# Kernel tuning notes

Hardware: AMD Instinct MI355X
Metric: run time of the kernel (lower is better)

Reference implementation:

```python
import jax, jax.numpy as jnp
import numpy as np

B, E, N = 8, 256, 32          # triples, padded edges per triple, neighbors per edge
D, RD = 512, 768              # graph_dim, relation-semantic dim
R = 2000                      # num relations
L = 2                         # relation-context layers
K = 8                         # top_k neighbor similarity
M, HEADS = 32, 8              # memory tokens, memory-attention heads
HLLM = 4096                   # llm hidden size
EPS = 1e-5


def _ln(x, g, b):
    mu = jnp.mean(x, -1, keepdims=True)
    var = jnp.mean(jnp.square(x - mu), -1, keepdims=True)
    return (x - mu) * jax.lax.rsqrt(var + EPS) * g + b


def setup_inputs() -> dict:
    key = jax.random.key(0)
    ks = iter(jax.random.split(key, 40))
    nrm = lambda shape, s=0.02: jax.random.normal(next(ks), shape, jnp.float32) * s
    return {
        'edge_rel_ids': jax.random.randint(next(ks), (B, E), 0, R, jnp.int32),
        'neighbor_rel_ids': jax.random.randint(next(ks), (B, E, N), 0, R, jnp.int32),
        'edge_mask': jnp.ones((B, E), jnp.float32),
        'rel_emb': nrm((R, RD), 1.0),
        'rp_w': nrm((D, RD)), 'rp_b': jnp.zeros((D,), jnp.float32),
        'ly_vw': nrm((L, D, D)), 'ly_vb': jnp.zeros((L, D), jnp.float32),
        'ly_ow': nrm((L, D, D)), 'ly_ob': jnp.zeros((L, D), jnp.float32),
        'ly_n1g': jnp.ones((L, D), jnp.float32), 'ly_n1b': jnp.zeros((L, D), jnp.float32),
        'ly_n2g': jnp.ones((L, D), jnp.float32), 'ly_n2b': jnp.zeros((L, D), jnp.float32),
        'ly_w1': nrm((L, 4 * D, D)), 'ly_b1': jnp.zeros((L, 4 * D), jnp.float32),
        'ly_w2': nrm((L, D, 4 * D)), 'ly_b2': jnp.zeros((L, D), jnp.float32),
        'mem_q': nrm((M, D)),
        't_qw': nrm((D, D)), 't_qb': jnp.zeros((D,), jnp.float32),
        't_kw': nrm((D, D)), 't_kb': jnp.zeros((D,), jnp.float32),
        't_vw': nrm((D, D)), 't_vb': jnp.zeros((D,), jnp.float32),
        't_ow': nrm((D, D)), 't_ob': jnp.zeros((D,), jnp.float32),
        'proj_w': nrm((HLLM, D)), 'proj_b': jnp.zeros((HLLM,), jnp.float32),
    }


def reference(edge_rel_ids, neighbor_rel_ids, edge_mask, rel_emb, rp_w, rp_b,
              ly_vw, ly_vb, ly_ow, ly_ob, ly_n1g, ly_n1b, ly_n2g, ly_n2b,
              ly_w1, ly_b1, ly_w2, ly_b2, mem_q,
              t_qw, t_qb, t_kw, t_kb, t_vw, t_vb, t_ow, t_ob, proj_w, proj_b):
    rel_vector = lambda ids: rel_emb[ids] @ rp_w.T + rp_b  # embedding gather + rel_proj
    rel_vec = rel_vector(edge_rel_ids)            # [B,E,D]
    neigh = rel_vector(neighbor_rel_ids)          # [B,E,N,D] dominant gather traffic
    # per-edge cosine similarity to neighbor relations, top-k mean aggregation
    rn = rel_vec / jnp.maximum(jnp.linalg.norm(rel_vec, axis=-1, keepdims=True), 1e-12)
    nn_ = neigh / jnp.maximum(jnp.linalg.norm(neigh, axis=-1, keepdims=True), 1e-12)
    sims = jnp.einsum('bend,bed->ben', nn_, rn)   # [B,E,N]
    _, top_idx = jax.lax.top_k(sims, K)           # [B,E,K]
    agg = jnp.take_along_axis(neigh, top_idx[..., None], axis=2).mean(axis=2)  # [B,E,D]
    # RelationContextLayer stack. Each layer attends from one edge-state token to a
    # single context token: softmax over one key is identically 1, so the MHA
    # reduces exactly to out_proj(v_proj(context)) -- same math as torch MHA here.
    states = rel_vec
    for l in range(L):
        attn = (agg @ ly_vw[l].T + ly_vb[l]) @ ly_ow[l].T + ly_ob[l]
        states = _ln(states + attn, ly_n1g[l], ly_n1b[l])
        ff = jax.nn.gelu(states @ ly_w1[l].T + ly_b1[l], approximate=False) @ ly_w2[l].T + ly_b2[l]
        states = _ln(states + ff, ly_n2g[l], ly_n2b[l])
        states = states * edge_mask[..., None]
    # GraphMemoryTokenizer: learned queries cross-attend over padded edge states
    dh = D // HEADS
    q = (mem_q @ t_qw.T + t_qb).reshape(M, HEADS, dh)
    k = (states @ t_kw.T + t_kb).reshape(B, E, HEADS, dh)
    v = (states @ t_vw.T + t_vb).reshape(B, E, HEADS, dh)
    scores = jnp.einsum('mhd,behd->bhme', q, k) / jnp.sqrt(jnp.asarray(dh, q.dtype))
    scores = jnp.where(edge_mask[:, None, None, :] == 0, jnp.finfo(scores.dtype).min, scores)
    attnw = jax.nn.softmax(scores, axis=-1)
    mem = jnp.einsum('bhme,behd->bmhd', attnw, v).reshape(B, M, D)
    mem = mem @ t_ow.T + t_ob
    no_edges = jnp.sum(edge_mask, axis=1) == 0    # rows with zero edges -> zero memory
    mem = jnp.where(no_edges[:, None, None], 0.0, mem)
    return mem @ proj_w.T + proj_b                # [B,M,HLLM]
```

## Files before the change

### kernel.cpp

```cpp
#include <hip/hip_runtime.h>
#include <hip/hip_bf16.h>
#include <math.h>

#define B_   8
#define E_   256
#define N_   32
#define D_   512
#define RD_  768
#define R_   2000
#define L_   2
#define K_   8
#define M_   32
#define H_   8
#define DH_  64
#define HL_  4096

typedef float f32x4 __attribute__((ext_vector_type(4)));
typedef __bf16 bf16x8 __attribute__((ext_vector_type(8)));
typedef const __attribute__((address_space(1))) void GVoid;
typedef __attribute__((address_space(3))) void LVoid;

__device__ __forceinline__ float gelu_exact(float x) {
    return 0.5f * x * (1.0f + erff(x * 0.70710678118654752f));
}
__device__ __forceinline__ unsigned short f2bf(float x) {
    return __hip_bfloat16_raw(__float2bfloat16(x)).x;
}

template <int TM, int TN, int ACT_GELU, int OUT_BF16, int HAS_BIAS, int FLAGS>
__global__ __launch_bounds__(256) void gemm_mfma(const unsigned short* __restrict__ A,
                                                 const unsigned short* __restrict__ W,
                                                 const float* __restrict__ bias,
                                                 void* __restrict__ Cv,
                                                 int M, int N, int K,
                                                 const float* __restrict__ rowflag) {
    constexpr int WTM = TM / 2, WTN = TN / 2;
    constexpr int RM = WTM / 16, RN = WTN / 16;
    constexpr int AI = TM / 32, BI = TN / 32;
    __shared__ __align__(16) unsigned short As[TM * 64];
    __shared__ __align__(16) unsigned short Bs[TN * 64];

    const int tid = threadIdx.x;
    const int wave = tid >> 6, lane = tid & 63;
    const int quad = lane >> 4, l16 = lane & 15;
    const int wm = wave >> 1, wn = wave & 1;
    const int bm = blockIdx.y * TM, bn = blockIdx.x * TN;
    const int sub = lane >> 3;
    const int cpr = (lane & 7) ^ sub;

    f32x4 acc[RM][RN];
#pragma unroll
    for (int i = 0; i < RM; i++)
#pragma unroll
        for (int j = 0; j < RN; j++) acc[i][j] = (f32x4){0.f, 0.f, 0.f, 0.f};

    for (int k0 = 0; k0 < K; k0 += 64) {
        __syncthreads();
#pragma unroll
        for (int i = 0; i < AI; i++) {
            int r0 = (wave * AI + i) * 8;
            const unsigned short* g = A + (size_t)(bm + r0 + sub) * K + k0 + cpr * 8;
            __builtin_amdgcn_global_load_lds((GVoid*)g, (LVoid*)&As[r0 * 64], 16, 0, 0);
        }
#pragma unroll
        for (int i = 0; i < BI; i++) {
            int r0 = (wave * BI + i) * 8;
            const unsigned short* g = W + (size_t)(bn + r0 + sub) * K + k0 + cpr * 8;
            __builtin_amdgcn_global_load_lds((GVoid*)g, (LVoid*)&Bs[r0 * 64], 16, 0, 0);
        }
        __syncthreads();
#pragma unroll
        for (int h = 0; h < 2; h++) {
            bf16x8 af[RM], bf[RN];
#pragma unroll
            for (int i = 0; i < RM; i++) {
                int r = wm * WTM + i * 16 + l16;
                int ch = (h * 4 + quad) ^ (r & 7);
                af[i] = *(const bf16x8*)&As[r * 64 + ch * 8];
            }
#pragma unroll
            for (int j = 0; j < RN; j++) {
                int r = wn * WTN + j * 16 + l16;
                int ch = (h * 4 + quad) ^ (r & 7);
                bf[j] = *(const bf16x8*)&Bs[r * 64 + ch * 8];
            }
#pragma unroll
            for (int i = 0; i < RM; i++)
#pragma unroll
                for (int j = 0; j < RN; j++)
                    acc[i][j] = __builtin_amdgcn_mfma_f32_16x16x32_bf16(af[i], bf[j], acc[i][j], 0, 0, 0);
        }
    }

#pragma unroll
    for (int i = 0; i < RM; i++) {
#pragma unroll
        for (int j = 0; j < RN; j++) {
            int c = bn + wn * WTN + j * 16 + l16;
            float bv = HAS_BIAS ? bias[c] : 0.f;
#pragma unroll
            for (int reg = 0; reg < 4; reg++) {
                int r = bm + wm * WTM + i * 16 + quad * 4 + reg;
                if (r < M) {
                    float v = acc[i][j][reg] + bv;
                    if (ACT_GELU) v = gelu_exact(v);
                    if (FLAGS) v *= rowflag[r >> 5];
                    if (OUT_BF16)
                        ((unsigned short*)Cv)[(size_t)r * N + c] = f2bf(v);
                    else
                        ((float*)Cv)[(size_t)r * N + c] = v;
                }
            }
        }
    }
}

__global__ __launch_bounds__(256) void projwfuse_kernel(
        const unsigned short* __restrict__ rel_bf, const unsigned short* __restrict__ rpw_bf,
        const float* __restrict__ rp_b, float* __restrict__ proj,
        const unsigned short* __restrict__ ow_bf, const unsigned short* __restrict__ vwT_bf,
        unsigned short* __restrict__ wfuse) {
    __shared__ __align__(16) unsigned short As[32 * 64];
    __shared__ __align__(16) unsigned short Bs[64 * 64];

    const unsigned short *A, *W;
    const float* bias;
    int Mg, Kg, bm, bn, obf;
    void* C;
    int t = blockIdx.x;
    if (t < 504) {
        A = rel_bf; W = rpw_bf; bias = rp_b; Mg = R_; Kg = RD_;
        C = proj; obf = 0; bn = (t & 7) * 64; bm = (t >> 3) * 32;
    } else {
        int u = t - 504, z = u >> 7, uu = u & 127;
        A = ow_bf + (size_t)z * 262144; W = vwT_bf + (size_t)z * 262144;
        bias = nullptr; Mg = 512; Kg = 512;
        C = wfuse + (size_t)z * 262144; obf = 1; bn = (uu & 7) * 64; bm = (uu >> 3) * 32;
    }

    const int tid = threadIdx.x;
    const int wave = tid >> 6, lane = tid & 63;
    const int quad = lane >> 4, l16 = lane & 15;
    const int wm = wave >> 1, wn = wave & 1;
    const int sub = lane >> 3;
    const int cpr = (lane & 7) ^ sub;

    f32x4 acc[2];
    acc[0] = (f32x4){0.f, 0.f, 0.f, 0.f};
    acc[1] = (f32x4){0.f, 0.f, 0.f, 0.f};

    for (int k0 = 0; k0 < Kg; k0 += 64) {
        __syncthreads();
        {
            int r0 = wave * 8;
            const unsigned short* g = A + (size_t)(bm + r0 + sub) * Kg + k0 + cpr * 8;
            __builtin_amdgcn_global_load_lds((GVoid*)g, (LVoid*)&As[r0 * 64], 16, 0, 0);
        }
#pragma unroll
        for (int i = 0; i < 2; i++) {
            int r0 = (wave * 2 + i) * 8;
            const unsigned short* g = W + (size_t)(bn + r0 + sub) * Kg + k0 + cpr * 8;
            __builtin_amdgcn_global_load_lds((GVoid*)g, (LVoid*)&Bs[r0 * 64], 16, 0, 0);
        }
        __syncthreads();
#pragma unroll
        for (int h = 0; h < 2; h++) {
            bf16x8 af, bf[2];
            {
                int r = wm * 16 + l16;
                int ch = (h * 4 + quad) ^ (r & 7);
                af = *(const bf16x8*)&As[r * 64 + ch * 8];
            }
#pragma unroll
            for (int j = 0; j < 2; j++) {
                int r = wn * 32 + j * 16 + l16;
                int ch = (h * 4 + quad) ^ (r & 7);
                bf[j] = *(const bf16x8*)&Bs[r * 64 + ch * 8];
            }
#pragma unroll
            for (int j = 0; j < 2; j++)
                acc[j] = __builtin_amdgcn_mfma_f32_16x16x32_bf16(af, bf[j], acc[j], 0, 0, 0);
        }
    }

#pragma unroll
    for (int j = 0; j < 2; j++) {
        int c = bn + wn * 32 + j * 16 + l16;
        float bv = bias ? bias[c] : 0.f;
#pragma unroll
        for (int reg = 0; reg < 4; reg++) {
            int r = bm + wm * 16 + quad * 4 + reg;
            if (r < Mg) {
                float v = acc[j][reg] + bv;
                if (obf)
                    ((unsigned short*)C)[(size_t)r * 512 + c] = f2bf(v);
                else
                    ((float*)C)[(size_t)r * 512 + c] = v;
            }
        }
    }
}

struct PrepArgs {
    const float* src[9];
    unsigned short* dst[9];
    int cum4[10];
    int nb_cvt, total4;
    const float* ly_vw; unsigned short* vwT;
    const float* ly_ow; const float* ly_vb; const float* ly_ob; float* bfuse;
    const float* t_kb; const float* t_vb; float* kvb;
    const float* edge_mask; float* flags;
    const float* mem_q; const float* t_qw; const float* t_qb; float* qbuf;
};

__global__ __launch_bounds__(256) void prep_all(PrepArgs a) {
    int bx = blockIdx.x, tid = threadIdx.x;
    if (bx < a.nb_cvt) {
        int i = bx * 256 + tid;
        if (i < a.total4) {
            int k = 0;
#pragma unroll
            for (int j = 0; j < 8; j++) if (i >= a.cum4[j + 1]) k = j + 1;
            int o = i - a.cum4[k];
            float4 v = ((const float4*)a.src[k])[o];
            ushort4 u;
            u.x = f2bf(v.x); u.y = f2bf(v.y); u.z = f2bf(v.z); u.w = f2bf(v.w);
            ((ushort4*)a.dst[k])[o] = u;
        }
        return;
    }
    bx -= a.nb_cvt;
    if (bx < 512) {
        __shared__ float tile[32][33];
        int l = bx >> 8, t16 = bx & 255;
        int j0 = (t16 >> 4) * 32, k0 = (t16 & 15) * 32;
        int tx = tid & 31, ty = tid >> 5;
        const float* src = a.ly_vw + (size_t)l * 512 * 512;
        for (int r = ty; r < 32; r += 8)
            tile[r][tx] = src[(size_t)(j0 + r) * 512 + k0 + tx];
        __syncthreads();
        unsigned short* dst = a.vwT + (size_t)l * 512 * 512;
        for (int r = ty; r < 32; r += 8)
            dst[(size_t)(k0 + r) * 512 + j0 + tx] = f2bf(tile[tx][r]);
        return;
    }
    bx -= 512;
    if (bx < 256) {
        int wid = bx * 4 + (tid >> 6);
        int z = wid >> 9, n = wid & 511, lane = tid & 63;
        const float* owr = a.ly_ow + (size_t)z * 512 * 512 + (size_t)n * 512;
        const float* vbr = a.ly_vb + (size_t)z * 512;
        float s = 0.f;
#pragma unroll
        for (int j = 0; j < 8; j++) s += owr[lane + 64 * j] * vbr[lane + 64 * j];
#pragma unroll
        for (int off = 32; off; off >>= 1) s += __shfl_xor(s, off, 64);
        if (lane == 0) a.bfuse[z * 512 + n] = s + a.ly_ob[z * 512 + n];
        return;
    }
    bx -= 256;
    if (bx < 1) {
        __shared__ float red[4];
        for (int n = tid; n < 512; n += 256) {
            a.kvb[n] = a.t_kb[n];
            a.kvb[n + 512] = a.t_vb[n];
        }
        for (int b = 0; b < B_; b++) {
            float s = a.edge_mask[b * E_ + tid];
#pragma unroll
            for (int off = 32; off; off >>= 1) s += __shfl_xor(s, off, 64);
            if ((tid & 63) == 0) red[tid >> 6] = s;
            __syncthreads();
            if (tid == 0)
                a.flags[b] = (red[0] + red[1] + red[2] + red[3] == 0.f) ? 0.f : 1.f;
            __syncthreads();
        }
        return;
    }
    bx -= 1;
    {
        int wid = bx * 4 + (tid >> 6);
        int m = wid >> 9, n = wid & 511, lane = tid & 63;
        const float* ar = a.mem_q + (size_t)m * 512;
        const float* br = a.t_qw + (size_t)n * 512;
        float s = 0.f;
#pragma unroll
        for (int j = 0; j < 8; j++) s += ar[lane + 64 * j] * br[lane + 64 * j];
#pragma unroll
        for (int off = 32; off; off >>= 1) s += __shfl_xor(s, off, 64);
        if (lane == 0) a.qbuf[(size_t)m * 512 + n] = s + a.t_qb[n];
    }
}

__global__ void sim_topk_agg(const int* __restrict__ eids, const int* __restrict__ nids,
                             const float* __restrict__ proj,
                             unsigned short* __restrict__ agg_bf, float* __restrict__ states) {
    int be = blockIdx.x, tid = threadIdx.x;
    __shared__ float ev[512];
    __shared__ float sims[32];
    __shared__ int nid_s[32];
    __shared__ int sel[8];

    int eid = eids[be];
    const float* ep = proj + (size_t)eid * D_;
    float e0 = ep[tid], e1 = ep[tid + 256];
    ev[tid] = e0; ev[tid + 256] = e1;
    states[(size_t)be * D_ + tid] = e0;
    states[(size_t)be * D_ + tid + 256] = e1;
    if (tid < 32) nid_s[tid] = nids[be * N_ + tid];
    __syncthreads();

    int wid = tid >> 6, lane = tid & 63;
    float se = 0.f;
#pragma unroll
    for (int j = 0; j < 8; j++) { float v = ev[lane + 64 * j]; se += v * v; }
#pragma unroll
    for (int off = 32; off; off >>= 1) se += __shfl_xor(se, off, 64);
    float en = fmaxf(sqrtf(se), 1e-12f);

    for (int n = wid; n < N_; n += 4) {
        int nid = nid_s[n];
        const float* np = proj + (size_t)nid * D_;
        float s = 0.f, s2 = 0.f;
#pragma unroll
        for (int j = 0; j < 8; j++) {
            float v = np[lane + 64 * j];
            s += v * ev[lane + 64 * j];
            s2 += v * v;
        }
#pragma unroll
        for (int off = 32; off; off >>= 1) {
            s += __shfl_xor(s, off, 64);
            s2 += __shfl_xor(s2, off, 64);
        }
        if (lane == 0) sims[n] = s / (fmaxf(sqrtf(s2), 1e-12f) * en);
    }
    __syncthreads();

    if (tid < 64) {
        float v = (tid < 32) ? sims[tid] : -3.402823466e38f;
        int idx = tid;
        for (int k = 0; k < K_; k++) {
            float bv = v; int bi = idx;
#pragma unroll
            for (int off = 32; off; off >>= 1) {
                float ov = __shfl_xor(bv, off, 64);
                int oi = __shfl_xor(bi, off, 64);
                if (ov > bv || (ov == bv && oi < bi)) { bv = ov; bi = oi; }
            }
            if (tid == 0) sel[k] = nid_s[bi];
            if (idx == bi) v = -3.402823466e38f;
        }
    }
    __syncthreads();

    float a0 = 0.f, a1 = 0.f;
#pragma unroll
    for (int k = 0; k < K_; k++) {
        const float* sp = proj + (size_t)sel[k] * D_;
        a0 += sp[tid]; a1 += sp[tid + 256];
    }
    agg_bf[(size_t)be * D_ + tid] = f2bf(a0 * 0.125f);
    agg_bf[(size_t)be * D_ + tid + 256] = f2bf(a1 * 0.125f);
}

__global__ void add_ln_kernel(const float* __restrict__ x, const float* __restrict__ y,
                              int ystride, const float* __restrict__ g,
                              const float* __restrict__ bb, const float* __restrict__ mask,
                              float* __restrict__ out, unsigned short* __restrict__ out_bf) {
    int t = blockIdx.x, tid = threadIdx.x;
    const float* xr = x + (size_t)t * D_;
    const float* yr = y + (size_t)t * ystride;
    float x0 = xr[tid] + yr[tid];
    float x1 = xr[tid + 256] + yr[tid + 256];
    __shared__ float red[8];
    float s = x0 + x1;
#pragma unroll
    for (int off = 32; off; off >>= 1) s += __shfl_xor(s, off, 64);
    int wid = tid >> 6;
    if ((tid & 63) == 0) red[wid] = s;
    __syncthreads();
    float mean = (red[0] + red[1] + red[2] + red[3]) * (1.f / 512.f);
    float d0 = x0 - mean, d1 = x1 - mean;
    float v = d0 * d0 + d1 * d1;
#pragma unroll
    for (int off = 32; off; off >>= 1) v += __shfl_xor(v, off, 64);
    if ((tid & 63) == 0) red[4 + wid] = v;
    __syncthreads();
    float var = (red[4] + red[5] + red[6] + red[7]) * (1.f / 512.f);
    float rs = rsqrtf(var + 1e-5f);
    float mv = mask ? mask[t] : 1.f;
    float o0 = (d0 * rs * g[tid] + bb[tid]) * mv;
    float o1 = (d1 * rs * g[tid + 256] + bb[tid + 256]) * mv;
    out[(size_t)t * D_ + tid] = o0;
    out[(size_t)t * D_ + tid + 256] = o1;
    out_bf[(size_t)t * D_ + tid] = f2bf(o0);
    out_bf[(size_t)t * D_ + tid + 256] = f2bf(o1);
}

__global__ void dbl_ln_kernel(const float* __restrict__ x, const float* __restrict__ y,
                              const float* __restrict__ g2, const float* __restrict__ b2,
                              const float* __restrict__ mask,
                              const float* __restrict__ att, int astride,
                              const float* __restrict__ g1, const float* __restrict__ b1,
                              float* __restrict__ out, unsigned short* __restrict__ out_bf) {
    int t = blockIdx.x, tid = threadIdx.x;
    const float* xr = x + (size_t)t * D_;
    const float* yr = y + (size_t)t * D_;
    float x0 = xr[tid] + yr[tid];
    float x1 = xr[tid + 256] + yr[tid + 256];
    __shared__ float red[8];
    int wid = tid >> 6;
    float s = x0 + x1;
#pragma unroll
    for (int off = 32; off; off >>= 1) s += __shfl_xor(s, off, 64);
    if ((tid & 63) == 0) red[wid] = s;
    __syncthreads();
    float mean = (red[0] + red[1] + red[2] + red[3]) * (1.f / 512.f);
    float d0 = x0 - mean, d1 = x1 - mean;
    float v = d0 * d0 + d1 * d1;
#pragma unroll
    for (int off = 32; off; off >>= 1) v += __shfl_xor(v, off, 64);
    if ((tid & 63) == 0) red[4 + wid] = v;
    __syncthreads();
    float var = (red[4] + red[5] + red[6] + red[7]) * (1.f / 512.f);
    float rs = rsqrtf(var + 1e-5f);
    float mv = mask[t];
    float t0 = (d0 * rs * g2[tid] + b2[tid]) * mv;
    float t1 = (d1 * rs * g2[tid + 256] + b2[tid + 256]) * mv;
    const float* ar = att + (size_t)t * astride;
    float y0 = t0 + ar[tid];
    float y1 = t1 + ar[tid + 256];
    __syncthreads();
    float s2 = y0 + y1;
#pragma unroll
    for (int off = 32; off; off >>= 1) s2 += __shfl_xor(s2, off, 64);
    if ((tid & 63) == 0) red[wid] = s2;
    __syncthreads();
    float mean2 = (red[0] + red[1] + red[2] + red[3]) * (1.f / 512.f);
    float e0 = y0 - mean2, e1 = y1 - mean2;
    float v2 = e0 * e0 + e1 * e1;
#pragma unroll
    for (int off = 32; off; off >>= 1) v2 += __shfl_xor(v2, off, 64);
    if ((tid & 63) == 0) red[4 + wid] = v2;
    __syncthreads();
    float var2 = (red[4] + red[5] + red[6] + red[7]) * (1.f / 512.f);
    float rs2 = rsqrtf(var2 + 1e-5f);
    float o0 = e0 * rs2 * g1[tid] + b1[tid];
    float o1 = e1 * rs2 * g1[tid + 256] + b1[tid + 256];
    out[(size_t)t * D_ + tid] = o0;
    out[(size_t)t * D_ + tid + 256] = o1;
    out_bf[(size_t)t * D_ + tid] = f2bf(o0);
    out_bf[(size_t)t * D_ + tid + 256] = f2bf(o1);
}

__global__ void mem_attn(const float* __restrict__ qb, const float* __restrict__ kv,
                         const float* __restrict__ mask, unsigned short* __restrict__ memb) {
    int idx = blockIdx.x;
    int b = idx & 7;
    int h = (idx >> 3) & 7;
    int m = idx >> 6;
    int tid = threadIdx.x;
    __shared__ float qh[64];
    __shared__ float sc[256];
    __shared__ float red[8];
    __shared__ float oacc[4][64];

    float mk = mask[b * E_ + tid];
    if (tid < 64) qh[tid] = qb[m * D_ + h * DH_ + tid];
    __syncthreads();
    const float* kr = kv + ((size_t)(b * E_ + tid)) * 1024 + h * DH_;
    float s = 0.f;
#pragma unroll
    for (int d = 0; d < DH_; d += 4) {
        float4 k4 = *(const float4*)(kr + d);
        s += k4.x * qh[d] + k4.y * qh[d + 1] + k4.z * qh[d + 2] + k4.w * qh[d + 3];
    }
    s *= 0.125f;
    if (mk == 0.f) s = -3.402823466e38f;
    float mx = s;
#pragma unroll
    for (int off = 32; off; off >>= 1) mx = fmaxf(mx, __shfl_xor(mx, off, 64));
    if ((tid & 63) == 0) red[tid >> 6] = mx;
    __syncthreads();
    mx = fmaxf(fmaxf(red[0], red[1]), fmaxf(red[2], red[3]));
    float p = expf(s - mx);
    float sum = p;
#pragma unroll
    for (int off = 32; off; off >>= 1) sum += __shfl_xor(sum, off, 64);
    if ((tid & 63) == 0) red[4 + (tid >> 6)] = sum;
    __syncthreads();
    sum = red[4] + red[5] + red[6] + red[7];
    sc[tid] = p / sum;
    __syncthreads();
    int d = tid & 63, part = tid >> 6;
    const float* vcol = kv + ((size_t)(b * E_ + part * 64)) * 1024 + 512 + h * DH_ + d;
    float acc = 0.f;
#pragma unroll 8
    for (int e = 0; e < 64; e++) acc += sc[part * 64 + e] * vcol[(size_t)e * 1024];
    oacc[part][d] = acc;
    __syncthreads();
    if (part == 0)
        memb[((size_t)(b * M_ + m)) * D_ + h * DH_ + d] =
            f2bf(oacc[0][d] + oacc[1][d] + oacc[2][d] + oacc[3][d]);
}

extern "C" void kernel_launch(void* const* d_in, const int* in_sizes, int n_in,
                              void* d_out, int out_size, void* d_ws, size_t ws_size,
                              hipStream_t stream) {
    const int*   edge_rel_ids     = (const int*)d_in[0];
    const int*   neighbor_rel_ids = (const int*)d_in[1];
    const float* edge_mask        = (const float*)d_in[2];
    const float* rel_emb          = (const float*)d_in[3];
    const float* rp_w             = (const float*)d_in[4];
    const float* rp_b             = (const float*)d_in[5];
    const float* ly_vw            = (const float*)d_in[6];
    const float* ly_vb            = (const float*)d_in[7];
    const float* ly_ow            = (const float*)d_in[8];
    const float* ly_ob            = (const float*)d_in[9];
    const float* ly_n1g           = (const float*)d_in[10];
    const float* ly_n1b           = (const float*)d_in[11];
    const float* ly_n2g           = (const float*)d_in[12];
    const float* ly_n2b           = (const float*)d_in[13];
    const float* ly_w1            = (const float*)d_in[14];
    const float* ly_b1            = (const float*)d_in[15];
    const float* ly_w2            = (const float*)d_in[16];
    const float* ly_b2            = (const float*)d_in[17];
    const float* mem_q            = (const float*)d_in[18];
    const float* t_qw             = (const float*)d_in[19];
    const float* t_qb             = (const float*)d_in[20];
    const float* t_kw             = (const float*)d_in[21];
    const float* t_kb             = (const float*)d_in[22];
    const float* t_vw             = (const float*)d_in[23];
    const float* t_vb             = (const float*)d_in[24];
    const float* t_ow             = (const float*)d_in[25];
    const float* t_ob             = (const float*)d_in[26];
    const float* proj_w           = (const float*)d_in[27];
    const float* proj_b           = (const float*)d_in[28];
    float* out = (float*)d_out;
    (void)ws_size; (void)in_sizes; (void)n_in; (void)out_size;

    char* ws = (char*)d_ws;
    size_t off = 0;
    auto allocf = [&](size_t n) { float* p = (float*)(ws + off); off += ((n * 4 + 255) & ~(size_t)255); return p; };
    auto allocb = [&](size_t n) { unsigned short* p = (unsigned short*)(ws + off); off += ((n * 2 + 255) & ~(size_t)255); return p; };

    const int T = B_ * E_;

    float* states  = allocf((size_t)T * D_);
    float* statesX = allocf((size_t)T * D_);
    float* proj    = allocf((size_t)R_ * D_);
    float* tmpB    = allocf((size_t)T * D_);
    float* attnall = allocf((size_t)T * 2 * D_);
    float* qbuf    = allocf((size_t)M_ * D_);
    float* bfuse   = allocf(2 * D_);
    float* kvb     = allocf(2 * D_);
    float* flags   = allocf(B_);
    float* kvbuf   = attnall;

    unsigned short* rel_bf  = allocb((size_t)2048 * RD_);
    unsigned short* rpw_bf  = allocb((size_t)D_ * RD_);
    unsigned short* agg_bf  = allocb((size_t)T * D_);
    unsigned short* st_bf   = allocb((size_t)T * D_);
    unsigned short* ff1_bf  = allocb((size_t)T * 4 * D_);
    unsigned short* vwT_bf  = allocb((size_t)L_ * D_ * D_);
    unsigned short* ow_bf   = allocb((size_t)L_ * D_ * D_);
    unsigned short* wfuse   = allocb((size_t)L_ * D_ * D_);
    unsigned short* w1_bf   = allocb((size_t)L_ * 4 * D_ * D_);
    unsigned short* w2_bf   = allocb((size_t)L_ * 4 * D_ * D_);
    unsigned short* kvw_bf  = allocb((size_t)2 * D_ * D_);
    unsigned short* tow_bf  = allocb((size_t)D_ * D_);
    unsigned short* pw_bf   = allocb((size_t)HL_ * D_);
    unsigned short* memb_bf = allocb((size_t)B_ * M_ * D_);
    unsigned short* mem2_bf = allocb((size_t)B_ * M_ * D_);

    PrepArgs a;
    int sizes[9] = { R_ * RD_, D_ * RD_, L_ * D_ * D_, L_ * 4 * D_ * D_,
                     L_ * 4 * D_ * D_, D_ * D_, D_ * D_, D_ * D_, HL_ * D_ };
    const float* srcs[9] = { rel_emb, rp_w, ly_ow, ly_w1, ly_w2, t_kw, t_vw, t_ow, proj_w };
    unsigned short* dsts[9] = { rel_bf, rpw_bf, ow_bf, w1_bf, w2_bf,
                                kvw_bf, kvw_bf + (size_t)D_ * D_, tow_bf, pw_bf };
    int cum = 0;
    for (int i = 0; i < 9; i++) {
        a.src[i] = srcs[i]; a.dst[i] = dsts[i];
        a.cum4[i] = cum; cum += sizes[i] / 4;
    }
    a.cum4[9] = cum;
    a.total4 = cum;
    a.nb_cvt = (cum + 255) / 256;
    a.ly_vw = ly_vw; a.vwT = vwT_bf;
    a.ly_ow = ly_ow; a.ly_vb = ly_vb; a.ly_ob = ly_ob; a.bfuse = bfuse;
    a.t_kb = t_kb; a.t_vb = t_vb; a.kvb = kvb;
    a.edge_mask = edge_mask; a.flags = flags;
    a.mem_q = mem_q; a.t_qw = t_qw; a.t_qb = t_qb; a.qbuf = qbuf;
    int nblk = a.nb_cvt + 512 + 256 + 1 + 4096;
    prep_all<<<nblk, 256, 0, stream>>>(a);

    projwfuse_kernel<<<760, 256, 0, stream>>>(rel_bf, rpw_bf, rp_b, proj,
                                              ow_bf, vwT_bf, wfuse);

    sim_topk_agg<<<T, 256, 0, stream>>>(edge_rel_ids, neighbor_rel_ids, proj,
                                        agg_bf, states);

    gemm_mfma<64, 64, 0, 0, 1, 0><<<dim3(16, 32), 256, 0, stream>>>(
        agg_bf, wfuse, bfuse, attnall, T, 2 * D_, D_, nullptr);

    add_ln_kernel<<<T, 256, 0, stream>>>(states, attnall, 2 * D_,
                                         ly_n1g, ly_n1b, nullptr, statesX, st_bf);
    gemm_mfma<64, 64, 1, 1, 1, 0><<<dim3(32, 32), 256, 0, stream>>>(
        st_bf, w1_bf, ly_b1, ff1_bf, T, 4 * D_, D_, nullptr);
    gemm_mfma<32, 64, 0, 0, 1, 0><<<dim3(8, 64), 256, 0, stream>>>(
        ff1_bf, w2_bf, ly_b2, tmpB, T, D_, 4 * D_, nullptr);
    dbl_ln_kernel<<<T, 256, 0, stream>>>(statesX, tmpB, ly_n2g, ly_n2b, edge_mask,
                                         attnall + D_, 2 * D_, ly_n1g + D_, ly_n1b + D_,
                                         states, st_bf);
    gemm_mfma<64, 64, 1, 1, 1, 0><<<dim3(32, 32), 256, 0, stream>>>(
        st_bf, w1_bf + (size_t)4 * D_ * D_, ly_b1 + 4 * D_, ff1_bf, T, 4 * D_, D_, nullptr);
    gemm_mfma<32, 64, 0, 0, 1, 0><<<dim3(8, 64), 256, 0, stream>>>(
        ff1_bf, w2_bf + (size_t)4 * D_ * D_, ly_b2 + D_, tmpB, T, D_, 4 * D_, nullptr);
    add_ln_kernel<<<T, 256, 0, stream>>>(states, tmpB, D_,
                                         ly_n2g + D_, ly_n2b + D_, edge_mask,
                                         statesX, st_bf);
    gemm_mfma<64, 64, 0, 0, 1, 0><<<dim3(16, 32), 256, 0, stream>>>(
        st_bf, kvw_bf, kvb, kvbuf, T, 2 * D_, D_, nullptr);
    mem_attn<<<B_ * M_ * H_, 256, 0, stream>>>(qbuf, kvbuf, edge_mask, memb_bf);
    gemm_mfma<32, 64, 0, 1, 1, 1><<<dim3(8, 8), 256, 0, stream>>>(
        memb_bf, tow_bf, t_ob, mem2_bf, B_ * M_, D_, D_, flags);
    gemm_mfma<32, 64, 0, 0, 1, 0><<<dim3(64, 8), 256, 0, stream>>>(
        mem2_bf, pw_bf, proj_b, out, B_ * M_, HL_, D_, nullptr);
}
```

Before: 310.3 us.

## Fuse memory cross-attention with output projection into one kernel per (batch, query)

Replaces the per-(b,h,m) mem_attn kernel plus the separate t_ow GEMM with a single attn_out kernel per (batch, memory token). Each of its four waves handles two heads: it computes the scores, the softmax and the V-weighted sum into a shared-memory row. The block then does the 512x512 output projection as bf16 dot products with wave reductions and applies bias and the no-edge flag. This removes one launch and the memb intermediate round trip. In exchange it drops from 2048 blocks to 256, serialises each wave over all 256 edges, and runs the output projection on scalar units instead of MFMA, so the per-block work is much longer.

```diff
diff --git a/kernel.cpp b/kernel.cpp
--- a/kernel.cpp
+++ b/kernel.cpp
@@ -27,13 +27,12 @@
     return __hip_bfloat16_raw(__float2bfloat16(x)).x;
 }
 
-template <int TM, int TN, int ACT_GELU, int OUT_BF16, int HAS_BIAS, int FLAGS>
+template <int TM, int TN, int ACT_GELU, int OUT_BF16, int HAS_BIAS>
 __global__ __launch_bounds__(256) void gemm_mfma(const unsigned short* __restrict__ A,
                                                  const unsigned short* __restrict__ W,
                                                  const float* __restrict__ bias,
                                                  void* __restrict__ Cv,
-                                                 int M, int N, int K,
-                                                 const float* __restrict__ rowflag) {
+                                                 int M, int N, int K) {
     constexpr int WTM = TM / 2, WTN = TN / 2;
     constexpr int RM = WTM / 16, RN = WTN / 16;
     constexpr int AI = TM / 32, BI = TN / 32;
@@ -104,7 +103,6 @@
                 if (r < M) {
                     float v = acc[i][j][reg] + bv;
                     if (ACT_GELU) v = gelu_exact(v);
-                    if (FLAGS) v *= rowflag[r >> 5];
                     if (OUT_BF16)
                         ((unsigned short*)Cv)[(size_t)r * N + c] = f2bf(v);
                     else
@@ -454,55 +452,83 @@
     out_bf[(size_t)t * D_ + tid + 256] = f2bf(o1);
 }
 
-__global__ void mem_attn(const float* __restrict__ qb, const float* __restrict__ kv,
-                         const float* __restrict__ mask, unsigned short* __restrict__ memb) {
-    int idx = blockIdx.x;
-    int b = idx & 7;
-    int h = (idx >> 3) & 7;
-    int m = idx >> 6;
+__global__ __launch_bounds__(256) void attn_out(
+        const float* __restrict__ qb, const float* __restrict__ kv,
+        const float* __restrict__ mask, const unsigned short* __restrict__ tow,
+        const float* __restrict__ t_ob, const float* __restrict__ flags,
+        unsigned short* __restrict__ mem2) {
+    int b = blockIdx.x & 7;
+    int m = blockIdx.x >> 3;
     int tid = threadIdx.x;
-    __shared__ float qh[64];
-    __shared__ float sc[256];
-    __shared__ float red[8];
-    __shared__ float oacc[4][64];
-
-    float mk = mask[b * E_ + tid];
-    if (tid < 64) qh[tid] = qb[m * D_ + h * DH_ + tid];
-    __syncthreads();
-    const float* kr = kv + ((size_t)(b * E_ + tid)) * 1024 + h * DH_;
-    float s = 0.f;
-#pragma unroll
-    for (int d = 0; d < DH_; d += 4) {
-        float4 k4 = *(const float4*)(kr + d);
-        s += k4.x * qh[d] + k4.y * qh[d + 1] + k4.z * qh[d + 2] + k4.w * qh[d + 3];
-    }
-    s *= 0.125f;
-    if (mk == 0.f) s = -3.402823466e38f;
-    float mx = s;
-#pragma unroll
-    for (int off = 32; off; off >>= 1) mx = fmaxf(mx, __shfl_xor(mx, off, 64));
-    if ((tid & 63) == 0) red[tid >> 6] = mx;
-    __syncthreads();
-    mx = fmaxf(fmaxf(red[0], red[1]), fmaxf(red[2], red[3]));
-    float p = expf(s - mx);
-    float sum = p;
-#pragma unroll
-    for (int off = 32; off; off >>= 1) sum += __shfl_xor(sum, off, 64);
-    if ((tid & 63) == 0) red[4 + (tid >> 6)] = sum;
-    __syncthreads();
-    sum = red[4] + red[5] + red[6] + red[7];
-    sc[tid] = p / sum;
-    __syncthreads();
-    int d = tid & 63, part = tid >> 6;
-    const float* vcol = kv + ((size_t)(b * E_ + part * 64)) * 1024 + 512 + h * DH_ + d;
-    float acc = 0.f;
+    int wave = tid >> 6, lane = tid & 63;
+    __shared__ float qh[512];
+    __shared__ float pbuf[4][256];
+    __shared__ float membrow[512];
+
+    qh[tid] = qb[(size_t)m * D_ + tid];
+    qh[tid + 256] = qb[(size_t)m * D_ + tid + 256];
+    __syncthreads();
+
+#pragma unroll
+    for (int hi = 0; hi < 2; hi++) {
+        int h = wave + hi * 4;
+        const float* qhp = &qh[h * DH_];
+        float sreg[4];
+#pragma unroll
+        for (int j = 0; j < 4; j++) {
+            int e = lane + j * 64;
+            const float* kr = kv + ((size_t)(b * E_ + e)) * 1024 + h * DH_;
+            float s = 0.f;
+#pragma unroll
+            for (int d = 0; d < DH_; d += 4) {
+                float4 k4 = *(const float4*)(kr + d);
+                s += k4.x * qhp[d] + k4.y * qhp[d + 1] + k4.z * qhp[d + 2] + k4.w * qhp[d + 3];
+            }
+            s *= 0.125f;
+            if (mask[b * E_ + e] == 0.f) s = -3.402823466e38f;
+            sreg[j] = s;
+        }
+        float mx = fmaxf(fmaxf(sreg[0], sreg[1]), fmaxf(sreg[2], sreg[3]));
+#pragma unroll
+        for (int off = 32; off; off >>= 1) mx = fmaxf(mx, __shfl_xor(mx, off, 64));
+        float sum = 0.f;
+#pragma unroll
+        for (int j = 0; j < 4; j++) { sreg[j] = expf(sreg[j] - mx); sum += sreg[j]; }
+#pragma unroll
+        for (int off = 32; off; off >>= 1) sum += __shfl_xor(sum, off, 64);
+        float inv = 1.f / sum;
+#pragma unroll
+        for (int j = 0; j < 4; j++) pbuf[wave][lane + j * 64] = sreg[j] * inv;
+        float acc = 0.f;
+        const float* vbase = kv + ((size_t)(b * E_)) * 1024 + 512 + h * DH_ + lane;
 #pragma unroll 8
-    for (int e = 0; e < 64; e++) acc += sc[part * 64 + e] * vcol[(size_t)e * 1024];
-    oacc[part][d] = acc;
-    __syncthreads();
-    if (part == 0)
-        memb[((size_t)(b * M_ + m)) * D_ + h * DH_ + d] =
-            f2bf(oacc[0][d] + oacc[1][d] + oacc[2][d] + oacc[3][d]);
+        for (int e = 0; e < E_; e++)
+            acc += pbuf[wave][e] * vbase[(size_t)e * 1024];
+        membrow[h * DH_ + lane] = acc;
+    }
+    __syncthreads();
+
+    float fl = flags[b];
+    float mreg[8];
+#pragma unroll
+    for (int j = 0; j < 8; j++) mreg[j] = membrow[lane * 8 + j];
+    for (int cc = 0; cc < 128; cc++) {
+        int c = wave * 128 + cc;
+        uint4 u = *(const uint4*)(tow + (size_t)c * 512 + lane * 8);
+        float part = 0.f;
+        part += __uint_as_float((u.x & 0xffffu) << 16) * mreg[0];
+        part += __uint_as_float(u.x & 0xffff0000u) * mreg[1];
+        part += __uint_as_float((u.y & 0xffffu) << 16) * mreg[2];
+        part += __uint_as_float(u.y & 0xffff0000u) * mreg[3];
+        part += __uint_as_float((u.z & 0xffffu) << 16) * mreg[4];
+        part += __uint_as_float(u.z & 0xffff0000u) * mreg[5];
+        part += __uint_as_float((u.w & 0xffffu) << 16) * mreg[6];
+        part += __uint_as_float(u.w & 0xffff0000u) * mreg[7];
+#pragma unroll
+        for (int off = 32; off; off >>= 1) part += __shfl_xor(part, off, 64);
+        if (lane == (c & 63))
+            mem2[((size_t)(b * M_ + m)) * D_ + c] = f2bf((part + t_ob[c]) * fl);
+    }
 }
 
 extern "C" void kernel_launch(void* const* d_in, const int* in_sizes, int n_in,
@@ -571,7 +597,6 @@
     unsigned short* kvw_bf  = allocb((size_t)2 * D_ * D_);
     unsigned short* tow_bf  = allocb((size_t)D_ * D_);
     unsigned short* pw_bf   = allocb((size_t)HL_ * D_);
-    unsigned short* memb_bf = allocb((size_t)B_ * M_ * D_);
     unsigned short* mem2_bf = allocb((size_t)B_ * M_ * D_);
 
     PrepArgs a;
@@ -602,30 +627,29 @@
     sim_topk_agg<<<T, 256, 0, stream>>>(edge_rel_ids, neighbor_rel_ids, proj,
                                         agg_bf, states);
 
-    gemm_mfma<64, 64, 0, 0, 1, 0><<<dim3(16, 32), 256, 0, stream>>>(
-        agg_bf, wfuse, bfuse, attnall, T, 2 * D_, D_, nullptr);
+    gemm_mfma<64, 64, 0, 0, 1><<<dim3(16, 32), 256, 0, stream>>>(
+        agg_bf, wfuse, bfuse, attnall, T, 2 * D_, D_);
 
     add_ln_kernel<<<T, 256, 0, stream>>>(states, attnall, 2 * D_,
                                          ly_n1g, ly_n1b, nullptr, statesX, st_bf);
-    gemm_mfma<64, 64, 1, 1, 1, 0><<<dim3(32, 32), 256, 0, stream>>>(
-        st_bf, w1_bf, ly_b1, ff1_bf, T, 4 * D_, D_, nullptr);
-    gemm_mfma<32, 64, 0, 0, 1, 0><<<dim3(8, 64), 256, 0, stream>>>(
-        ff1_bf, w2_bf, ly_b2, tmpB, T, D_, 4 * D_, nullptr);
+    gemm_mfma<64, 64, 1, 1, 1><<<dim3(32, 32), 256, 0, stream>>>(
+        st_bf, w1_bf, ly_b1, ff1_bf, T, 4 * D_, D_);
+    gemm_mfma<32, 64, 0, 0, 1><<<dim3(8, 64), 256, 0, stream>>>(
+        ff1_bf, w2_bf, ly_b2, tmpB, T, D_, 4 * D_);
     dbl_ln_kernel<<<T, 256, 0, stream>>>(statesX, tmpB, ly_n2g, ly_n2b, edge_mask,
                                          attnall + D_, 2 * D_, ly_n1g + D_, ly_n1b + D_,
                                          states, st_bf);
-    gemm_mfma<64, 64, 1, 1, 1, 0><<<dim3(32, 32), 256, 0, stream>>>(
-        st_bf, w1_bf + (size_t)4 * D_ * D_, ly_b1 + 4 * D_, ff1_bf, T, 4 * D_, D_, nullptr);
-    gemm_mfma<32, 64, 0, 0, 1, 0><<<dim3(8, 64), 256, 0, stream>>>(
-        ff1_bf, w2_bf + (size_t)4 * D_ * D_, ly_b2 + D_, tmpB, T, D_, 4 * D_, nullptr);
+    gemm_mfma<64, 64, 1, 1, 1><<<dim3(32, 32), 256, 0, stream>>>(
+        st_bf, w1_bf + (size_t)4 * D_ * D_, ly_b1 + 4 * D_, ff1_bf, T, 4 * D_, D_);
+    gemm_mfma<32, 64, 0, 0, 1><<<dim3(8, 64), 256, 0, stream>>>(
+        ff1_bf, w2_bf + (size_t)4 * D_ * D_, ly_b2 + D_, tmpB, T, D_, 4 * D_);
     add_ln_kernel<<<T, 256, 0, stream>>>(states, tmpB, D_,
                                          ly_n2g + D_, ly_n2b + D_, edge_mask,
                                          statesX, st_bf);
-    gemm_mfma<64, 64, 0, 0, 1, 0><<<dim3(16, 32), 256, 0, stream>>>(
-        st_bf, kvw_bf, kvb, kvbuf, T, 2 * D_, D_, nullptr);
-    mem_attn<<<B_ * M_ * H_, 256, 0, stream>>>(qbuf, kvbuf, edge_mask, memb_bf);
-    gemm_mfma<32, 64, 0, 1, 1, 1><<<dim3(8, 8), 256, 0, stream>>>(
-        memb_bf, tow_bf, t_ob, mem2_bf, B_ * M_, D_, D_, flags);
-    gemm_mfma<32, 64, 0, 0, 1, 0><<<dim3(64, 8), 256, 0, stream>>>(
-        mem2_bf, pw_bf, proj_b, out, B_ * M_, HL_, D_, nullptr);
-}
+    gemm_mfma<64, 64, 0, 0, 1><<<dim3(16, 32), 256, 0, stream>>>(
+        st_bf, kvw_bf, kvb, kvbuf, T, 2 * D_, D_);
+    attn_out<<<B_ * M_, 256, 0, stream>>>(qbuf, kvbuf, edge_mask, tow_bf, t_ob,
+                                          flags, mem2_bf);
+    gemm_mfma<32, 64, 0, 0, 1><<<dim3(64, 8), 256, 0, stream>>>(
+        mem2_bf, pw_bf, proj_b, out, B_ * M_, HL_, D_);
+}
```

Result: slower. 399.9 us (+28.9%).
